# Kernel optimization log

Hardware: AMD Instinct MI355X
Metric: run time of the kernel (lower is better)

## Reference

```python
import jax, jax.numpy as jnp
import numpy as np

EPS = 1e-7  # SimplifiedLayerNorm eps


def setup_inputs() -> dict:
    key = jax.random.key(0)
    k1, k2 = jax.random.split(key)
    x = jax.random.normal(k1, (8, 2048, 64), dtype=jnp.float32)   # [B, T, d]
    W = jax.random.normal(k2, (2048, 8), dtype=jnp.float32)       # [T, H] per-distance, per-head Toeplitz weights
    return {"x": x, "W": W}


def _l2norm(v):
    return v / (jnp.linalg.norm(v, axis=-1, keepdims=True) + EPS)


def reference(x, W):
    B, T, d = x.shape
    H = W.shape[1]
    # pad one zero token: [B, T+1, d]
    xp = jnp.concatenate([x, jnp.zeros((B, 1, d), x.dtype)], axis=1)
    idx = jnp.arange(T + 1)
    dist = idx[:, None] - idx[None, :]                 # [T+1, T+1], row - col
    # Toeplitz logits: W[dist, h] for 0 <= dist < T; the single dist==T entry
    # (bottom-left corner) is left at its initial 0.0; dist < 0 is causally masked.
    Wd = W[jnp.clip(dist, 0, T - 1)]                   # [T+1, T+1, H]
    dist3 = dist[..., None]
    logits = jnp.where(dist3 < 0, -jnp.inf,
                       jnp.where(dist3 >= T, jnp.zeros((), x.dtype), Wd))
    probs = jax.nn.softmax(logits, axis=1)             # softmax over columns (dim=-1 of W_h)
    v = jnp.einsum('tsh,bsd->hbtd', probs, xp)         # [H, B, T+1, d]
    v = _l2norm(v)
    V = jnp.concatenate([v, xp[None]], axis=0)         # [H+1, B, T+1, d]
    V = _l2norm(V)
    return V
```

## Files before the change

### kernel.cpp

```cpp
#include <hip/hip_runtime.h>

#define EPS 1e-7f
#define T_DIM 2048
#define TP1   2049
#define H_DIM 8
#define B_DIM 8
#define SP    2080
#define NFRAG 138
#define FB_OFF 32
#define RSTRIDE 66

typedef short v8s __attribute__((ext_vector_type(8)));
typedef float v4f __attribute__((ext_vector_type(4)));

static __device__ __forceinline__ unsigned short f2bf(float f) {
  union { float f; unsigned u; } v; v.f = f;
  unsigned r = v.u + 0x7fffu + ((v.u >> 16) & 1u);
  return (unsigned short)(r >> 16);
}

#define J1_BLOCKS 276
#define J2_BLOCKS 264
#define J3_BLOCKS 4098

__global__ __launch_bounds__(256) void prep(const float* __restrict__ x,
                                            const float* __restrict__ W,
                                            unsigned short* __restrict__ fragA,
                                            unsigned short* __restrict__ xT,
                                            float* __restrict__ out) {
  __shared__ float tile[64][65];
  int bid = blockIdx.x;
  if (bid < J1_BLOCKS) {
    int tid = bid * 256 + threadIdx.x;
    int blk = tid >> 6, lane = tid & 63;
    int h = blk / NFRAG, fb = blk - h * NFRAG;
    int b0 = fb * 16 - FB_OFF;
    int lm = lane & 15, quad = lane >> 4;
    v8s frag;
    #pragma unroll
    for (int j = 0; j < 8; ++j) {
      int d = b0 + lm - 8 * quad - j;
      float v = 0.0f;
      if (d >= 0 && d < T_DIM) v = __expf(W[d * H_DIM + h]);
      else if (d == T_DIM) v = 1.0f;
      frag[j] = (short)f2bf(v);
    }
    *(v8s*)(fragA + (size_t)tid * 8) = frag;
    return;
  }
  bid -= J1_BLOCKS;
  if (bid < J2_BLOCKS) {
    int b = bid / 33, st = bid % 33;
    int tid = threadIdx.x;
    if (st == 32) {
      #pragma unroll
      for (int i = 0; i < 8; ++i) {
        int idx = tid * 8 + i;
        int dd = idx >> 5, sl = idx & 31;
        xT[((size_t)b * 64 + dd) * SP + T_DIM + sl] = 0;
      }
      return;
    }
    int s0 = st * 64;
    int c = tid & 63, r4 = tid >> 6;
    #pragma unroll
    for (int i = 0; i < 16; ++i) {
      int sl = r4 * 16 + i;
      tile[sl][c] = x[((size_t)b * T_DIM + (s0 + sl)) * 64 + c];
    }
    __syncthreads();
    #pragma unroll
    for (int i = 0; i < 16; ++i) {
      int dd = r4 * 16 + i;
      xT[((size_t)b * 64 + dd) * SP + s0 + c] = f2bf(tile[c][dd]);
    }
    return;
  }
  bid -= J2_BLOCKS;
  {
    int row = bid * 4 + (threadIdx.x >> 6);
    if (row >= B_DIM * TP1) return;
    int b = row / TP1, t = row - b * TP1;
    int dd = threadIdx.x & 63;
    float v = (t < T_DIM) ? x[((size_t)b * T_DIM + t) * 64 + dd] : 0.0f;
    float ss = v * v;
    ss += __shfl_xor(ss, 1);  ss += __shfl_xor(ss, 2);
    ss += __shfl_xor(ss, 4);  ss += __shfl_xor(ss, 8);
    ss += __shfl_xor(ss, 16); ss += __shfl_xor(ss, 32);
    float inv = 1.0f / (sqrtf(ss) + EPS);
    __builtin_nontemporal_store(v * inv,
        &out[(((size_t)(H_DIM * B_DIM + b) * TP1 + t) << 6) + dd]);
  }
}

__global__ __launch_bounds__(256) void toeplitz_mm(const unsigned short* __restrict__ fragA,
                                                   const unsigned short* __restrict__ xT,
                                                   float* __restrict__ out) {
  __shared__ float red[2][64 * RSTRIDE];

  const int lane = threadIdx.x & 63;
  const int w    = threadIdx.x >> 6;
  const int wm   = w & 1;
  const int wk   = w >> 1;
  const int lm   = lane & 15;
  const int quad = lane >> 4;

  const int bi  = blockIdx.x;
  const int tb  = 16 - (bi >> 6);
  const int rem = bi & 63;
  const int h = rem & 7, b = (rem >> 3) & 7;
  const int t0 = tb * 128;
  const int tw = t0 + 64 * wm;

  const unsigned short* fA = fragA + ((size_t)h * NFRAG * 64 + lane) * 8;
  const unsigned short* xb = xT + ((size_t)b * 64 + lm) * SP + 8 * quad;

  const int sw_end = min(tw + 32, T_DIM);

  v4f acc[4][4] = {};

  v8s a0[4], a1[4], b0[4], b1[4];

#define LOAD_A(dst, s0v) do {                                        \
    const v8s* _p = (const v8s*)(fA + (size_t)((tw - (s0v) + FB_OFF) >> 4) * 512); \
    dst[0] = _p[0]; dst[1] = _p[64]; dst[2] = _p[128]; dst[3] = _p[192]; } while (0)
#define LOAD_B(dst, s0v) do {                                        \
    const unsigned short* _p = xb + (s0v);                           \
    dst[0] = *(const v8s*)(_p);                                      \
    dst[1] = *(const v8s*)(_p + 16 * SP);                            \
    dst[2] = *(const v8s*)(_p + 32 * SP);                            \
    dst[3] = *(const v8s*)(_p + 48 * SP); } while (0)
#define DO_MFMA(fa, fb) do {                                         \
    _Pragma("unroll")                                                \
    for (int mt = 0; mt < 4; ++mt)                                   \
      _Pragma("unroll")                                              \
      for (int nt = 0; nt < 4; ++nt)                                 \
        acc[mt][nt] = __builtin_amdgcn_mfma_f32_16x16x32_bf16(fa[mt], fb[nt], acc[mt][nt], 0, 0, 0); } while (0)

  int s0 = 32 * wk;
  LOAD_A(a0, s0); LOAD_B(b0, s0);
  for (;;) {
    bool more = (s0 + 64 <= sw_end);
    if (more) { LOAD_A(a1, s0 + 64); LOAD_B(b1, s0 + 64); }
    DO_MFMA(a0, b0);
    if (!more) break;
    s0 += 64;
    bool more2 = (s0 + 64 <= sw_end);
    if (more2) { LOAD_A(a0, s0 + 64); LOAD_B(b0, s0 + 64); }
    DO_MFMA(a1, b1);
    if (!more2) break;
    s0 += 64;
  }

  if (wk == 1) {
    float* buf = red[wm];
    #pragma unroll
    for (int mt = 0; mt < 4; ++mt)
      #pragma unroll
      for (int r = 0; r < 4; ++r) {
        int row = 16 * mt + 4 * quad + r;
        #pragma unroll
        for (int nt = 0; nt < 4; ++nt)
          buf[row * RSTRIDE + 16 * nt + lm] = acc[mt][nt][r];
      }
  }
  __syncthreads();
  if (wk != 0) return;

  const float* buf = red[wm];
  #pragma unroll
  for (int mt = 0; mt < 4; ++mt) {
    #pragma unroll
    for (int r = 0; r < 4; ++r) {
      int row = 16 * mt + 4 * quad + r;
      #pragma unroll
      for (int nt = 0; nt < 4; ++nt)
        acc[mt][nt][r] += buf[row * RSTRIDE + 16 * nt + lm];
    }
  }

  #pragma unroll
  for (int mt = 0; mt < 4; ++mt) {
    #pragma unroll
    for (int r = 0; r < 4; ++r) {
      float ss = 0.0f;
      #pragma unroll
      for (int nt = 0; nt < 4; ++nt) { float a = acc[mt][nt][r]; ss += a * a; }
      ss += __shfl_xor(ss, 1);
      ss += __shfl_xor(ss, 2);
      ss += __shfl_xor(ss, 4);
      ss += __shfl_xor(ss, 8);
      int t = tw + 16 * mt + 4 * quad + r;
      if (t <= T_DIM) {
        float n1 = sqrtf(ss);
        float u  = n1 / (n1 + EPS);
        float inv = 1.0f / ((n1 + EPS) * (u + EPS));
        float* op = out + (((size_t)(h * B_DIM + b) * TP1 + t) << 6) + lm;
        #pragma unroll
        for (int nt = 0; nt < 4; ++nt)
          __builtin_nontemporal_store(acc[mt][nt][r] * inv, op + 16 * nt);
      }
    }
  }
}

extern "C" void kernel_launch(void* const* d_in, const int* in_sizes, int n_in,
                              void* d_out, int out_size, void* d_ws, size_t ws_size,
                              hipStream_t stream) {
  const float* x = (const float*)d_in[0];
  const float* W = (const float*)d_in[1];
  float* out = (float*)d_out;

  unsigned short* xT    = (unsigned short*)d_ws;
  unsigned short* fragA = (unsigned short*)((char*)d_ws + 2131968);

  hipLaunchKernelGGL(prep, dim3(J1_BLOCKS + J2_BLOCKS + J3_BLOCKS), dim3(256), 0, stream,
                     x, W, fragA, xT, out);
  hipLaunchKernelGGL(toeplitz_mm, dim3(64 * 17), dim3(256), 0, stream, fragA, xT, out);
}
```

Baseline: 114.6 us.

## Stage Toeplitz and x tiles through LDS with async double buffering

The matmul kernel now stages A fragments and swizzled bf16 x tiles into shared memory with global_load_lds, double-buffered, instead of each wave loading fragments from global memory directly. Each block shares one A stream across two batches and drops the split-K LDS reduction. The x-normalization pass moves from the prep kernel into the matmul launch as extra blocks, so prep gets smaller and that work overlaps the GEMM tail. It adds barriers per stage and changes the block decomposition, which risks load imbalance across levels.

Result: faster. 103.7 us (-9.5%).

```diff
diff --git a/kernel.cpp b/kernel.cpp
--- a/kernel.cpp
+++ b/kernel.cpp
@@ -5,10 +5,16 @@
 #define TP1   2049
 #define H_DIM 8
 #define B_DIM 8
-#define SP    2080
-#define NFRAG 138
-#define FB_OFF 32
-#define RSTRIDE 66
+
+#define NFRAG 146
+#define NST   33
+#define AREG  10240
+#define BUFSZ 26624
+
+#define J1_BLOCKS 292
+#define J2_BLOCKS 264
+#define MM_BLOCKS 544
+#define J3_BLOCKS 4098
 
 typedef short v8s __attribute__((ext_vector_type(8)));
 typedef float v4f __attribute__((ext_vector_type(4)));
@@ -19,22 +25,23 @@
   return (unsigned short)(r >> 16);
 }
 
-#define J1_BLOCKS 276
-#define J2_BLOCKS 264
-#define J3_BLOCKS 4098
+static __device__ __forceinline__ void load_lds16(const void* g, void* l) {
+  __builtin_amdgcn_global_load_lds(
+      (const __attribute__((address_space(1))) unsigned int*)g,
+      (__attribute__((address_space(3))) unsigned int*)l, 16, 0, 0);
+}
 
 __global__ __launch_bounds__(256) void prep(const float* __restrict__ x,
                                             const float* __restrict__ W,
                                             unsigned short* __restrict__ fragA,
-                                            unsigned short* __restrict__ xT,
-                                            float* __restrict__ out) {
+                                            unsigned short* __restrict__ xT) {
   __shared__ float tile[64][65];
   int bid = blockIdx.x;
   if (bid < J1_BLOCKS) {
     int tid = bid * 256 + threadIdx.x;
     int blk = tid >> 6, lane = tid & 63;
-    int h = blk / NFRAG, fb = blk - h * NFRAG;
-    int b0 = fb * 16 - FB_OFF;
+    int h = blk / NFRAG, fbp = blk - h * NFRAG;
+    int b0 = fbp * 16 - 160;
     int lm = lane & 15, quad = lane >> 4;
     v8s frag;
     #pragma unroll
@@ -49,37 +56,41 @@
     return;
   }
   bid -= J1_BLOCKS;
-  if (bid < J2_BLOCKS) {
-    int b = bid / 33, st = bid % 33;
+  {
+    int b = bid / NST, st = bid - b * NST;
+    int s0 = st * 64;
     int tid = threadIdx.x;
-    if (st == 32) {
-      #pragma unroll
-      for (int i = 0; i < 8; ++i) {
-        int idx = tid * 8 + i;
-        int dd = idx >> 5, sl = idx & 31;
-        xT[((size_t)b * 64 + dd) * SP + T_DIM + sl] = 0;
-      }
-      return;
-    }
-    int s0 = st * 64;
     int c = tid & 63, r4 = tid >> 6;
     #pragma unroll
     for (int i = 0; i < 16; ++i) {
       int sl = r4 * 16 + i;
-      tile[sl][c] = x[((size_t)b * T_DIM + (s0 + sl)) * 64 + c];
+      int s = s0 + sl;
+      tile[sl][c] = (s < T_DIM) ? x[((size_t)b * T_DIM + s) * 64 + c] : 0.0f;
     }
     __syncthreads();
-    #pragma unroll
-    for (int i = 0; i < 16; ++i) {
-      int dd = r4 * 16 + i;
-      xT[((size_t)b * 64 + dd) * SP + s0 + c] = f2bf(tile[c][dd]);
-    }
-    return;
-  }
-  bid -= J2_BLOCKS;
-  {
-    int row = bid * 4 + (threadIdx.x >> 6);
-    if (row >= B_DIM * TP1) return;
+    int dd = tid >> 2, pb = (tid & 3) * 2;
+    unsigned short* dst = xT + ((size_t)(b * NST + st) << 12) + dd * 64;
+    #pragma unroll
+    for (int e = 0; e < 2; ++e) {
+      int p = pb + e;
+      int sb = ((p ^ (dd & 7)) << 3);
+      v8s o;
+      #pragma unroll
+      for (int j = 0; j < 8; ++j) o[j] = (short)f2bf(tile[sb + j][dd]);
+      *(v8s*)(dst + p * 8) = o;
+    }
+  }
+}
+
+__global__ __launch_bounds__(256) void toeplitz_mm(const float* __restrict__ x,
+                                                   const unsigned short* __restrict__ fragA,
+                                                   const unsigned short* __restrict__ xT,
+                                                   float* __restrict__ out) {
+  __shared__ __align__(16) char smem[2][BUFSZ];
+
+  int bid = blockIdx.x;
+  if (bid >= MM_BLOCKS) {
+    int row = (bid - MM_BLOCKS) * 4 + (threadIdx.x >> 6);
     int b = row / TP1, t = row - b * TP1;
     int dd = threadIdx.x & 63;
     float v = (t < T_DIM) ? x[((size_t)b * T_DIM + t) * 64 + dd] : 0.0f;
@@ -90,94 +101,81 @@
     float inv = 1.0f / (sqrtf(ss) + EPS);
     __builtin_nontemporal_store(v * inv,
         &out[(((size_t)(H_DIM * B_DIM + b) * TP1 + t) << 6) + dd]);
-  }
-}
-
-__global__ __launch_bounds__(256) void toeplitz_mm(const unsigned short* __restrict__ fragA,
-                                                   const unsigned short* __restrict__ xT,
-                                                   float* __restrict__ out) {
-  __shared__ float red[2][64 * RSTRIDE];
+    return;
+  }
 
   const int lane = threadIdx.x & 63;
   const int w    = threadIdx.x >> 6;
   const int wm   = w & 1;
-  const int wk   = w >> 1;
+  const int wb   = w >> 1;
   const int lm   = lane & 15;
   const int quad = lane >> 4;
 
-  const int bi  = blockIdx.x;
-  const int tb  = 16 - (bi >> 6);
-  const int rem = bi & 63;
-  const int h = rem & 7, b = (rem >> 3) & 7;
-  const int t0 = tb * 128;
-  const int tw = t0 + 64 * wm;
-
-  const unsigned short* fA = fragA + ((size_t)h * NFRAG * 64 + lane) * 8;
-  const unsigned short* xb = xT + ((size_t)b * 64 + lm) * SP + 8 * quad;
-
-  const int sw_end = min(tw + 32, T_DIM);
+  const int h   = bid & 7;
+  const int bg  = (bid >> 3) & 3;
+  const int lvl = bid >> 5;
+  const int t0  = T_DIM - lvl * 128;
+  const int tw  = t0 + 64 * wm;
+  const int b   = bg * 2 + wb;
+  const bool active = (tw <= T_DIM);
+  const int cap = tw + 32;
+
+  const int NS = (min(t0 + 96, T_DIM) >> 6) + 1;
+
+  const unsigned short* fA = fragA + (size_t)h * NFRAG * 512 + lane * 8;
+
+#define STAGE(bufi, it) do {                                                   \
+    int _s0 = (it) << 6;                                                       \
+    int _E0p = ((t0 - _s0 + 32) >> 4) + 6;                                     \
+    const unsigned short* _A = fA + (size_t)_E0p * 512;                        \
+    const unsigned short* _B = xT + ((size_t)((bg * 2) * NST + (_s0 >> 6)) << 12) + lane * 8; \
+    char* _lb = &smem[bufi][0];                                                \
+    _Pragma("unroll")                                                          \
+    for (int _i = 0; _i < 7; ++_i) {                                           \
+      int _u = w + _i * 4;                                                     \
+      if (_u < 26) {                                                           \
+        const unsigned short* _src = (_u < 10)                                 \
+            ? (_A + (size_t)_u * 512)                                          \
+            : (_B + (((_u - 10) >> 3) * (NST * 4096)) + (((_u - 10) & 7) * 512)); \
+        load_lds16(_src, _lb + _u * 1024);                                     \
+      }                                                                        \
+    }                                                                          \
+  } while (0)
 
   v4f acc[4][4] = {};
 
-  v8s a0[4], a1[4], b0[4], b1[4];
-
-#define LOAD_A(dst, s0v) do {                                        \
-    const v8s* _p = (const v8s*)(fA + (size_t)((tw - (s0v) + FB_OFF) >> 4) * 512); \
-    dst[0] = _p[0]; dst[1] = _p[64]; dst[2] = _p[128]; dst[3] = _p[192]; } while (0)
-#define LOAD_B(dst, s0v) do {                                        \
-    const unsigned short* _p = xb + (s0v);                           \
-    dst[0] = *(const v8s*)(_p);                                      \
-    dst[1] = *(const v8s*)(_p + 16 * SP);                            \
-    dst[2] = *(const v8s*)(_p + 32 * SP);                            \
-    dst[3] = *(const v8s*)(_p + 48 * SP); } while (0)
-#define DO_MFMA(fa, fb) do {                                         \
-    _Pragma("unroll")                                                \
-    for (int mt = 0; mt < 4; ++mt)                                   \
-      _Pragma("unroll")                                              \
-      for (int nt = 0; nt < 4; ++nt)                                 \
-        acc[mt][nt] = __builtin_amdgcn_mfma_f32_16x16x32_bf16(fa[mt], fb[nt], acc[mt][nt], 0, 0, 0); } while (0)
-
-  int s0 = 32 * wk;
-  LOAD_A(a0, s0); LOAD_B(b0, s0);
-  for (;;) {
-    bool more = (s0 + 64 <= sw_end);
-    if (more) { LOAD_A(a1, s0 + 64); LOAD_B(b1, s0 + 64); }
-    DO_MFMA(a0, b0);
-    if (!more) break;
-    s0 += 64;
-    bool more2 = (s0 + 64 <= sw_end);
-    if (more2) { LOAD_A(a0, s0 + 64); LOAD_B(b0, s0 + 64); }
-    DO_MFMA(a1, b1);
-    if (!more2) break;
-    s0 += 64;
-  }
-
-  if (wk == 1) {
-    float* buf = red[wm];
-    #pragma unroll
-    for (int mt = 0; mt < 4; ++mt)
-      #pragma unroll
-      for (int r = 0; r < 4; ++r) {
-        int row = 16 * mt + 4 * quad + r;
+  STAGE(0, 0);
+  __syncthreads();
+  int buf = 0;
+  for (int it = 0; it < NS; ++it) {
+    if (it + 1 < NS) STAGE(buf ^ 1, it + 1);
+    const char* Ab = &smem[buf][0];
+    const char* Bb = Ab + AREG + wb * 8192;
+    int s0 = it << 6;
+    #pragma unroll
+    for (int kk = 0; kk < 2; ++kk) {
+      if (active && (s0 + 32 * kk <= cap)) {
+        v8s af[4], bf[4];
+        #pragma unroll
+        for (int mt = 0; mt < 4; ++mt)
+          af[mt] = *(const v8s*)(Ab + (2 + 4 * wm - 2 * kk + mt) * 1024 + lane * 16);
         #pragma unroll
         for (int nt = 0; nt < 4; ++nt)
-          buf[row * RSTRIDE + 16 * nt + lm] = acc[mt][nt][r];
+          bf[nt] = *(const v8s*)(Bb + nt * 2048 + lm * 128 +
+                                 ((((kk << 2) | quad) ^ (lm & 7)) << 4));
+        #pragma unroll
+        for (int mt = 0; mt < 4; ++mt)
+          #pragma unroll
+          for (int nt = 0; nt < 4; ++nt)
+            acc[mt][nt] = __builtin_amdgcn_mfma_f32_16x16x32_bf16(af[mt], bf[nt],
+                                                                  acc[mt][nt], 0, 0, 0);
       }
-  }
-  __syncthreads();
-  if (wk != 0) return;
-
-  const float* buf = red[wm];
-  #pragma unroll
-  for (int mt = 0; mt < 4; ++mt) {
-    #pragma unroll
-    for (int r = 0; r < 4; ++r) {
-      int row = 16 * mt + 4 * quad + r;
-      #pragma unroll
-      for (int nt = 0; nt < 4; ++nt)
-        acc[mt][nt][r] += buf[row * RSTRIDE + 16 * nt + lm];
-    }
-  }
+    }
+    __syncthreads();
+    buf ^= 1;
+  }
+
+  if (!active) return;
 
   #pragma unroll
   for (int mt = 0; mt < 4; ++mt) {
@@ -202,6 +200,7 @@
       }
     }
   }
+#undef STAGE
 }
 
 extern "C" void kernel_launch(void* const* d_in, const int* in_sizes, int n_in,
@@ -212,9 +211,10 @@
   float* out = (float*)d_out;
 
   unsigned short* xT    = (unsigned short*)d_ws;
-  unsigned short* fragA = (unsigned short*)((char*)d_ws + 2131968);
-
-  hipLaunchKernelGGL(prep, dim3(J1_BLOCKS + J2_BLOCKS + J3_BLOCKS), dim3(256), 0, stream,
-                     x, W, fragA, xT, out);
-  hipLaunchKernelGGL(toeplitz_mm, dim3(64 * 17), dim3(256), 0, stream, fragA, xT, out);
-}
+  unsigned short* fragA = (unsigned short*)((char*)d_ws + 2162688);
+
+  hipLaunchKernelGGL(prep, dim3(J1_BLOCKS + J2_BLOCKS), dim3(256), 0, stream,
+                     x, W, fragA, xT);
+  hipLaunchKernelGGL(toeplitz_mm, dim3(MM_BLOCKS + J3_BLOCKS), dim3(256), 0, stream,
+                     x, fragA, xT, out);
+}
```
